# Kernel optimization log

Measured on AMD Instinct MI355X. Metric: run time of the kernel, lower is better.

Reference implementation:

```python
import jax, jax.numpy as jnp
import numpy as np

N_NODES = 100000


def gcn_conv(x, W, b, src, dst, n):
    # PyG GCNConv: add self-loops, symmetric deg^{-1/2} normalization,
    # h = x @ W, out[i] = sum_j norm_ij * h[j] + b
    loop = jnp.arange(n, dtype=src.dtype)
    s = jnp.concatenate([src, loop])
    d = jnp.concatenate([dst, loop])
    h = x @ W  # [N, F_out]
    deg = jax.ops.segment_sum(jnp.ones_like(d, dtype=x.dtype), d, num_segments=n)
    dinv = jnp.where(deg > 0, jax.lax.rsqrt(deg), 0.0)
    norm = dinv[s] * dinv[d]  # [E+N]
    msgs = h[s] * norm[:, None]  # gather + scale
    out = jax.ops.segment_sum(msgs, d, num_segments=n)  # scatter-add
    return out + b


def setup_inputs() -> dict:
    key = jax.random.key(0)
    ks = jax.random.split(key, 8)
    n, e = N_NODES, 1600000
    return {
        "clinical": jax.random.normal(ks[0], (n, 64), dtype=jnp.float32),
        "mel": jax.random.normal(ks[1], (n, 1024), dtype=jnp.float32),
        "edge_index": jax.random.randint(ks[2], (2, e), 0, n, dtype=jnp.int64),
        "W_mel": jax.random.normal(ks[3], (1024, 128), dtype=jnp.float32) * 0.03,
        "b_mel": jnp.zeros((128,), dtype=jnp.float32),
        "W_cat": jax.random.normal(ks[4], (192, 128), dtype=jnp.float32) * 0.07,
        "b_cat": jnp.zeros((128,), dtype=jnp.float32),
        "W1": jax.random.normal(ks[5], (128, 128), dtype=jnp.float32) * 0.09,
        "b1": jnp.zeros((128,), dtype=jnp.float32),
        "W2": jax.random.normal(ks[6], (128, 4), dtype=jnp.float32) * 0.09,
        "b2": jnp.zeros((4,), dtype=jnp.float32),
    }


def reference(clinical, mel, edge_index, W_mel, b_mel, W_cat, b_cat, W1, b1, W2, b2):
    n = clinical.shape[0]
    src, dst = edge_index[0], edge_index[1]
    m = jax.nn.relu(mel @ W_mel + b_mel)            # [N, 128]
    x = jnp.concatenate([clinical, m], axis=1)       # [N, 192]
    x = jax.nn.relu(x @ W_cat + b_cat)               # [N, 128]
    x = jax.nn.relu(gcn_conv(x, W1, b1, src, dst, n))
    x = gcn_conv(x, W2, b2, src, dst, n)             # [N, 4]
    return x
```

## Files before the change

kernel.cpp:

```cpp
#include <hip/hip_runtime.h>
#include <cstdint>


__device__ __forceinline__ bool detect_i64(const int* __restrict__ ei) {
  int nz = 0;
#pragma unroll
  for (int i = 1; i < 64; i += 2) nz |= ei[i];
  return nz == 0;
}
__device__ __forceinline__ int load_src(const int* __restrict__ ei, int e, bool is64) {
  return is64 ? ei[2 * e] : ei[e];
}
__device__ __forceinline__ int load_dst(const int* __restrict__ ei, int e, int E, bool is64) {
  return is64 ? ei[2 * (E + e)] : ei[E + e];
}

__global__ __launch_bounds__(256) void zero_int_k(int* __restrict__ p, int n) {
  int i = blockIdx.x * 256 + threadIdx.x;
  if (i < n) p[i] = 0;
}

__global__ __launch_bounds__(256) void count_deg_k(const int* __restrict__ ei,
                                                   int* __restrict__ degi, int E) {
  const bool is64 = detect_i64(ei);
  int e = blockIdx.x * 256 + threadIdx.x;
  if (e < E) atomicAdd(&degi[load_dst(ei, e, E, is64)], 1);
}

__global__ __launch_bounds__(256) void dinv_k(const int* __restrict__ degi,
                                              float* __restrict__ dinv, int n) {
  int i = blockIdx.x * 256 + threadIdx.x;
  if (i < n) dinv[i] = rsqrtf((float)degi[i] + 1.0f);
}

__global__ __launch_bounds__(256) void scan_reduce_k(const int* __restrict__ degi,
                                                     int* __restrict__ partial, int n) {
  __shared__ int s[256];
  int t = threadIdx.x;
  int i = blockIdx.x * 256 + t;
  s[t] = (i < n) ? degi[i] : 0;
  __syncthreads();
#pragma unroll
  for (int off = 128; off > 0; off >>= 1) {
    if (t < off) s[t] += s[t + off];
    __syncthreads();
  }
  if (t == 0) partial[blockIdx.x] = s[0];
}

__global__ __launch_bounds__(512) void scan_partials_k(const int* __restrict__ partial,
                                                       int* __restrict__ excl, int B,
                                                       int* __restrict__ rowptr, int n, int E) {
  __shared__ int s[512];
  int t = threadIdx.x;
  int v = (t < B) ? partial[t] : 0;
  s[t] = v;
  __syncthreads();
  for (int off = 1; off < 512; off <<= 1) {
    int x = (t >= off) ? s[t - off] : 0;
    __syncthreads();
    s[t] += x;
    __syncthreads();
  }
  if (t < B) excl[t] = s[t] - v;
  if (t == 0) rowptr[n] = E;
}

__global__ __launch_bounds__(256) void scan_final_k(const int* __restrict__ degi,
                                                    const int* __restrict__ excl,
                                                    int* __restrict__ rowptr, int n) {
  __shared__ int s[256];
  int t = threadIdx.x;
  int i = blockIdx.x * 256 + t;
  int v = (i < n) ? degi[i] : 0;
  s[t] = v;
  __syncthreads();
  for (int off = 1; off < 256; off <<= 1) {
    int x = (t >= off) ? s[t - off] : 0;
    __syncthreads();
    s[t] += x;
    __syncthreads();
  }
  if (i < n) rowptr[i] = excl[blockIdx.x] + s[t] - v;
}

__global__ __launch_bounds__(256) void fill_col_k(const int* __restrict__ ei,
                                                  const int* __restrict__ rowptr,
                                                  int* __restrict__ fill,
                                                  int* __restrict__ col, int E) {
  const bool is64 = detect_i64(ei);
  int e = blockIdx.x * 256 + threadIdx.x;
  if (e < E) {
    int s = load_src(ei, e, is64);
    int d = load_dst(ei, e, E, is64);
    int pos = rowptr[d] + atomicAdd(&fill[d], 1);
    col[pos] = s;
  }
}

template <bool RELU, bool HASBIAS>
__global__ __launch_bounds__(256) void gemm128_k(const float* __restrict__ A, int K,
                                                 const float* __restrict__ B,
                                                 const float* __restrict__ bias,
                                                 float* __restrict__ C, int n) {
  __shared__ float As[64][33];
  __shared__ float4 Bs[32][32];
  const int tid = threadIdx.x;
  const int tx = tid & 31, ty = tid >> 5;
  const int row0 = blockIdx.x * 64;
  float acc[8][4];
#pragma unroll
  for (int i = 0; i < 8; ++i)
#pragma unroll
    for (int j = 0; j < 4; ++j) acc[i][j] = 0.f;

  const int nChunks = K >> 5;
  for (int kc = 0; kc < nChunks; ++kc) {
    __syncthreads();
#pragma unroll
    for (int j = 0; j < 2; ++j) {
      int idx = tid + j * 256;
      int ar = idx >> 3, ac4 = idx & 7;
      int grow = row0 + ar;
      float4 v = make_float4(0.f, 0.f, 0.f, 0.f);
      if (grow < n) v = *(const float4*)(A + (size_t)grow * K + kc * 32 + ac4 * 4);
      As[ar][ac4 * 4 + 0] = v.x;
      As[ar][ac4 * 4 + 1] = v.y;
      As[ar][ac4 * 4 + 2] = v.z;
      As[ar][ac4 * 4 + 3] = v.w;
    }
#pragma unroll
    for (int j = 0; j < 4; ++j) {
      int idx = tid + j * 256;
      int br = idx >> 5, bc4 = idx & 31;
      Bs[br][bc4] = *(const float4*)(B + (size_t)(kc * 32 + br) * 128 + bc4 * 4);
    }
    __syncthreads();
#pragma unroll
    for (int kk = 0; kk < 32; ++kk) {
      float4 b = Bs[kk][tx];
#pragma unroll
      for (int i = 0; i < 8; ++i) {
        float a = As[ty * 8 + i][kk];
        acc[i][0] += a * b.x;
        acc[i][1] += a * b.y;
        acc[i][2] += a * b.z;
        acc[i][3] += a * b.w;
      }
    }
  }
  float4 bb = make_float4(0.f, 0.f, 0.f, 0.f);
  if (HASBIAS) bb = *(const float4*)(bias + tx * 4);
#pragma unroll
  for (int i = 0; i < 8; ++i) {
    int grow = row0 + ty * 8 + i;
    if (grow < n) {
      float4 o;
      o.x = acc[i][0] + bb.x;
      o.y = acc[i][1] + bb.y;
      o.z = acc[i][2] + bb.z;
      o.w = acc[i][3] + bb.w;
      if (RELU) {
        o.x = fmaxf(o.x, 0.f);
        o.y = fmaxf(o.y, 0.f);
        o.z = fmaxf(o.z, 0.f);
        o.w = fmaxf(o.w, 0.f);
      }
      *(float4*)(C + (size_t)grow * 128 + tx * 4) = o;
    }
  }
}

__global__ __launch_bounds__(256) void gemm_cat_k(const float* __restrict__ A1,
                                                  const float* __restrict__ A2,
                                                  const float* __restrict__ B,
                                                  const float* __restrict__ bias,
                                                  float* __restrict__ C, int n) {
  __shared__ float As[64][33];
  __shared__ float4 Bs[32][32];
  const int tid = threadIdx.x;
  const int tx = tid & 31, ty = tid >> 5;
  const int row0 = blockIdx.x * 64;
  float acc[8][4];
#pragma unroll
  for (int i = 0; i < 8; ++i)
#pragma unroll
    for (int j = 0; j < 4; ++j) acc[i][j] = 0.f;

  for (int kc = 0; kc < 6; ++kc) {
    __syncthreads();
#pragma unroll
    for (int j = 0; j < 2; ++j) {
      int idx = tid + j * 256;
      int ar = idx >> 3, ac4 = idx & 7;
      int grow = row0 + ar;
      int kcol = kc * 32 + ac4 * 4;
      float4 v = make_float4(0.f, 0.f, 0.f, 0.f);
      if (grow < n) {
        v = (kcol < 64) ? *(const float4*)(A1 + (size_t)grow * 64 + kcol)
                        : *(const float4*)(A2 + (size_t)grow * 128 + (kcol - 64));
      }
      As[ar][ac4 * 4 + 0] = v.x;
      As[ar][ac4 * 4 + 1] = v.y;
      As[ar][ac4 * 4 + 2] = v.z;
      As[ar][ac4 * 4 + 3] = v.w;
    }
#pragma unroll
    for (int j = 0; j < 4; ++j) {
      int idx = tid + j * 256;
      int br = idx >> 5, bc4 = idx & 31;
      Bs[br][bc4] = *(const float4*)(B + (size_t)(kc * 32 + br) * 128 + bc4 * 4);
    }
    __syncthreads();
#pragma unroll
    for (int kk = 0; kk < 32; ++kk) {
      float4 b = Bs[kk][tx];
#pragma unroll
      for (int i = 0; i < 8; ++i) {
        float a = As[ty * 8 + i][kk];
        acc[i][0] += a * b.x;
        acc[i][1] += a * b.y;
        acc[i][2] += a * b.z;
        acc[i][3] += a * b.w;
      }
    }
  }
  float4 bb = *(const float4*)(bias + tx * 4);
#pragma unroll
  for (int i = 0; i < 8; ++i) {
    int grow = row0 + ty * 8 + i;
    if (grow < n) {
      float4 o;
      o.x = fmaxf(acc[i][0] + bb.x, 0.f);
      o.y = fmaxf(acc[i][1] + bb.y, 0.f);
      o.z = fmaxf(acc[i][2] + bb.z, 0.f);
      o.w = fmaxf(acc[i][3] + bb.w, 0.f);
      *(float4*)(C + (size_t)grow * 128 + tx * 4) = o;
    }
  }
}

template <bool RELU>
__global__ __launch_bounds__(256) void gather128_k(const int* __restrict__ col,
                                                   const int* __restrict__ rowptr,
                                                   const float* __restrict__ dinv,
                                                   const float* __restrict__ h,
                                                   const float* __restrict__ bias,
                                                   float* __restrict__ out, int n) {
  const int node = blockIdx.x * 2 + (threadIdx.x >> 7);
  const int f = threadIdx.x & 127;
  if (node >= n) return;
  const int beg = rowptr[node], end = rowptr[node + 1];
  float acc = 0.f;
  int p = beg;
  for (; p + 4 <= end; p += 4) {
    int s0 = col[p], s1 = col[p + 1], s2 = col[p + 2], s3 = col[p + 3];
    float d0 = dinv[s0], d1 = dinv[s1], d2 = dinv[s2], d3 = dinv[s3];
    float h0 = h[(size_t)s0 * 128 + f];
    float h1 = h[(size_t)s1 * 128 + f];
    float h2 = h[(size_t)s2 * 128 + f];
    float h3 = h[(size_t)s3 * 128 + f];
    acc += d0 * h0 + d1 * h1 + d2 * h2 + d3 * h3;
  }
  for (; p < end; ++p) {
    int s = col[p];
    acc += dinv[s] * h[(size_t)s * 128 + f];
  }
  const float di = dinv[node];
  float v = di * (acc + di * h[(size_t)node * 128 + f]) + bias[f];
  if (RELU) v = fmaxf(v, 0.f);
  out[(size_t)node * 128 + f] = v;
}

__global__ __launch_bounds__(256) void gemm_small4_k(const float* __restrict__ A,
                                                     const float* __restrict__ W,
                                                     float* __restrict__ Y, int n) {
  __shared__ float Ws[512];
  int tid = threadIdx.x;
  Ws[tid] = W[tid];
  Ws[tid + 256] = W[tid + 256];
  __syncthreads();
  int row = blockIdx.x * 256 + tid;
  if (row >= n) return;
  const float4* A4 = (const float4*)(A + (size_t)row * 128);
  float a0 = 0.f, a1 = 0.f, a2 = 0.f, a3 = 0.f;
#pragma unroll
  for (int k4 = 0; k4 < 32; ++k4) {
    float4 a = A4[k4];
    const float* w = &Ws[k4 * 16];
    a0 += a.x * w[0] + a.y * w[4] + a.z * w[8] + a.w * w[12];
    a1 += a.x * w[1] + a.y * w[5] + a.z * w[9] + a.w * w[13];
    a2 += a.x * w[2] + a.y * w[6] + a.z * w[10] + a.w * w[14];
    a3 += a.x * w[3] + a.y * w[7] + a.z * w[11] + a.w * w[15];
  }
  *(float4*)(Y + (size_t)row * 4) = make_float4(a0, a1, a2, a3);
}

__global__ __launch_bounds__(256) void gather4_k(const int* __restrict__ col,
                                                 const int* __restrict__ rowptr,
                                                 const float* __restrict__ dinv,
                                                 const float* __restrict__ y,
                                                 const float* __restrict__ b2,
                                                 float* __restrict__ out, int n) {
  int node = blockIdx.x * 256 + threadIdx.x;
  if (node >= n) return;
  const int beg = rowptr[node], end = rowptr[node + 1];
  float ax = 0.f, ay = 0.f, az = 0.f, aw = 0.f;
  int p = beg;
  for (; p + 2 <= end; p += 2) {
    int s0 = col[p], s1 = col[p + 1];
    float d0 = dinv[s0], d1 = dinv[s1];
    float4 y0 = *(const float4*)(y + (size_t)s0 * 4);
    float4 y1 = *(const float4*)(y + (size_t)s1 * 4);
    ax += d0 * y0.x + d1 * y1.x;
    ay += d0 * y0.y + d1 * y1.y;
    az += d0 * y0.z + d1 * y1.z;
    aw += d0 * y0.w + d1 * y1.w;
  }
  for (; p < end; ++p) {
    int s = col[p];
    float ds = dinv[s];
    float4 yv = *(const float4*)(y + (size_t)s * 4);
    ax += ds * yv.x;
    ay += ds * yv.y;
    az += ds * yv.z;
    aw += ds * yv.w;
  }
  const float di = dinv[node];
  float4 yd = *(const float4*)(y + (size_t)node * 4);
  float4 o;
  o.x = di * (ax + di * yd.x) + b2[0];
  o.y = di * (ay + di * yd.y) + b2[1];
  o.z = di * (az + di * yd.z) + b2[2];
  o.w = di * (aw + di * yd.w) + b2[3];
  *(float4*)(out + (size_t)node * 4) = o;
}

extern "C" void kernel_launch(void* const* d_in, const int* in_sizes, int n_in,
                              void* d_out, int out_size, void* d_ws, size_t ws_size,
                              hipStream_t stream) {
  const float* clinical = (const float*)d_in[0];
  const float* mel = (const float*)d_in[1];
  const int* ei = (const int*)d_in[2];
  const float* W_mel = (const float*)d_in[3];
  const float* b_mel = (const float*)d_in[4];
  const float* W_cat = (const float*)d_in[5];
  const float* b_cat = (const float*)d_in[6];
  const float* W1 = (const float*)d_in[7];
  const float* b1 = (const float*)d_in[8];
  const float* W2 = (const float*)d_in[9];
  const float* b2 = (const float*)d_in[10];
  float* out = (float*)d_out;

  const int N = in_sizes[0] / 64;
  const int E = in_sizes[2] / 2;
  const int B = (N + 255) / 256;

  float* bufA = (float*)d_ws;
  float* bufB = bufA + (size_t)N * 128;
  float* dinv = bufB + (size_t)N * 128;
  float* ybuf = dinv + N;
  int* degi = (int*)(ybuf + (size_t)N * 4);
  int* rowptr = degi + N;
  int* fill = rowptr + (N + 1);
  int* partial = fill + N;
  int* excl = partial + 512;
  int* col = excl + 512;

  const dim3 blk(256);

  zero_int_k<<<(2 * N + 255) / 256, blk, 0, stream>>>(degi, 2 * N);
  count_deg_k<<<(E + 255) / 256, blk, 0, stream>>>(ei, degi, E);
  dinv_k<<<B, blk, 0, stream>>>(degi, dinv, N);
  scan_reduce_k<<<B, blk, 0, stream>>>(degi, partial, N);
  scan_partials_k<<<1, 512, 0, stream>>>(partial, excl, B, rowptr, N, E);
  scan_final_k<<<B, blk, 0, stream>>>(degi, excl, rowptr, N);
  zero_int_k<<<B, blk, 0, stream>>>(fill, N);
  fill_col_k<<<(E + 255) / 256, blk, 0, stream>>>(ei, rowptr, fill, col, E);

  gemm128_k<true, true><<<(N + 63) / 64, blk, 0, stream>>>(mel, 1024, W_mel, b_mel, bufA, N);
  gemm_cat_k<<<(N + 63) / 64, blk, 0, stream>>>(clinical, bufA, W_cat, b_cat, bufB, N);
  gemm128_k<false, false><<<(N + 63) / 64, blk, 0, stream>>>(bufB, 128, W1, nullptr, bufA, N);

  gather128_k<true><<<(N + 1) / 2, blk, 0, stream>>>(col, rowptr, dinv, bufA, b1, bufB, N);

  gemm_small4_k<<<(N + 255) / 256, blk, 0, stream>>>(bufB, W2, ybuf, N);

  gather4_k<<<(N + 255) / 256, blk, 0, stream>>>(col, rowptr, dinv, ybuf, b2, out, N);
}
```

Baseline: 1.311 ms.

## Use bf16 MFMA for the large mel projection GEMM

Replaces the scalar fp32 mel@W_mel GEMM with a bf16 MFMA kernel. A and W are converted to bf16 on the fly, and W is pre-transposed by a small conversion kernel. The aim is to remove the compute bottleneck of the 1024-wide projection while reading A once per 128-row tile. The cost is reduced input precision (bf16 rounding), with fp32 accumulation kept.

```diff
diff --git a/kernel.cpp b/kernel.cpp
--- a/kernel.cpp
+++ b/kernel.cpp
@@ -1,6 +1,17 @@
 #include <hip/hip_runtime.h>
 #include <cstdint>
 
+
+typedef short short4_t __attribute__((ext_vector_type(4)));
+typedef short short8_t __attribute__((ext_vector_type(8)));
+typedef float floatx4 __attribute__((ext_vector_type(4)));
+
+__device__ __forceinline__ short f2bf(float f) {
+  union { float f; unsigned u; } v;
+  v.f = f;
+  unsigned r = v.u + 0x7fffu + ((v.u >> 16) & 1u);
+  return (short)(r >> 16);
+}
 
 __device__ __forceinline__ bool detect_i64(const int* __restrict__ ei) {
   int nz = 0;
@@ -95,6 +106,90 @@
     int d = load_dst(ei, e, E, is64);
     int pos = rowptr[d] + atomicAdd(&fill[d], 1);
     col[pos] = s;
+  }
+}
+
+__global__ __launch_bounds__(256) void convW_k(const float* __restrict__ W,
+                                               short* __restrict__ Wt) {
+  int idx = blockIdx.x * 256 + threadIdx.x;
+  int nn = idx >> 10;
+  int k = idx & 1023;
+  Wt[idx] = f2bf(W[(size_t)k * 128 + nn]);
+}
+
+__global__ __launch_bounds__(256) void mel_gemm_mfma_k(const float* __restrict__ A,
+                                                       const short* __restrict__ Wt,
+                                                       const float* __restrict__ bias,
+                                                       float* __restrict__ C, int n) {
+  __shared__ short Asm[128][72];
+  __shared__ short Bsm[128][72];
+  const int tid = threadIdx.x;
+  const int row0 = blockIdx.x * 128;
+  const int lane = tid & 63;
+  const int wv = tid >> 6;
+  const int quad = lane >> 4;
+  const int cbase = lane & 15;
+
+  floatx4 acc[2][8];
+#pragma unroll
+  for (int tr = 0; tr < 2; ++tr)
+#pragma unroll
+    for (int tc = 0; tc < 8; ++tc) acc[tr][tc] = (floatx4){0.f, 0.f, 0.f, 0.f};
+
+  for (int kc = 0; kc < 16; ++kc) {
+    __syncthreads();
+#pragma unroll
+    for (int j = 0; j < 8; ++j) {
+      int idx = j * 256 + tid;
+      int row = idx >> 4, c4 = idx & 15;
+      int grow = row0 + row;
+      floatx4 v = (floatx4){0.f, 0.f, 0.f, 0.f};
+      if (grow < n) v = *(const floatx4*)(A + (size_t)grow * 1024 + kc * 64 + c4 * 4);
+      short4_t s4;
+      s4[0] = f2bf(v[0]); s4[1] = f2bf(v[1]); s4[2] = f2bf(v[2]); s4[3] = f2bf(v[3]);
+      *(short4_t*)&Asm[row][c4 * 4] = s4;
+    }
+#pragma unroll
+    for (int j = 0; j < 8; ++j) {
+      int idx = j * 256 + tid;
+      int nr = idx >> 4, c4 = idx & 15;
+      *(short4_t*)&Bsm[nr][c4 * 4] =
+          *(const short4_t*)(Wt + (size_t)nr * 1024 + kc * 64 + c4 * 4);
+    }
+    __syncthreads();
+#pragma unroll
+    for (int kk = 0; kk < 2; ++kk) {
+      short8_t af[2], bf[8];
+#pragma unroll
+      for (int tr = 0; tr < 2; ++tr)
+        af[tr] = *(const short8_t*)&Asm[wv * 32 + tr * 16 + cbase][kk * 32 + quad * 8];
+#pragma unroll
+      for (int tc = 0; tc < 8; ++tc)
+        bf[tc] = *(const short8_t*)&Bsm[tc * 16 + cbase][kk * 32 + quad * 8];
+#pragma unroll
+      for (int tr = 0; tr < 2; ++tr)
+#pragma unroll
+        for (int tc = 0; tc < 8; ++tc)
+          acc[tr][tc] = __builtin_amdgcn_mfma_f32_16x16x32_bf16(af[tr], bf[tc],
+                                                                acc[tr][tc], 0, 0, 0);
+    }
+  }
+  float bb[8];
+#pragma unroll
+  for (int tc = 0; tc < 8; ++tc) bb[tc] = bias[tc * 16 + cbase];
+#pragma unroll
+  for (int tr = 0; tr < 2; ++tr) {
+#pragma unroll
+    for (int r = 0; r < 4; ++r) {
+      int grow = row0 + wv * 32 + tr * 16 + quad * 4 + r;
+      if (grow < n) {
+#pragma unroll
+        for (int tc = 0; tc < 8; ++tc) {
+          float v = acc[tr][tc][r] + bb[tc];
+          C[(size_t)grow * 128 + tc * 16 + cbase] = fmaxf(v, 0.f);
+        }
+      }
+    }
   }
 }
 
@@ -366,10 +461,11 @@
   int* partial = fill + N;
   int* excl = partial + 512;
   int* col = excl + 512;
+  short* Wt = (short*)(col + E);
 
   const dim3 blk(256);
 
-  zero_int_k<<<(2 * N + 255) / 256, blk, 0, stream>>>(degi, 2 * N);
+  zero_int_k<<<(N + 255) / 256, blk, 0, stream>>>(degi, N);
   count_deg_k<<<(E + 255) / 256, blk, 0, stream>>>(ei, degi, E);
   dinv_k<<<B, blk, 0, stream>>>(degi, dinv, N);
   scan_reduce_k<<<B, blk, 0, stream>>>(degi, partial, N);
@@ -377,8 +473,9 @@
   scan_final_k<<<B, blk, 0, stream>>>(degi, excl, rowptr, N);
   zero_int_k<<<B, blk, 0, stream>>>(fill, N);
   fill_col_k<<<(E + 255) / 256, blk, 0, stream>>>(ei, rowptr, fill, col, E);
-
-  gemm128_k<true, true><<<(N + 63) / 64, blk, 0, stream>>>(mel, 1024, W_mel, b_mel, bufA, N);
+  convW_k<<<512, blk, 0, stream>>>(W_mel, Wt);
+
+  mel_gemm_mfma_k<<<(N + 127) / 128, blk, 0, stream>>>(mel, Wt, b_mel, bufA, N);
   gemm_cat_k<<<(N + 63) / 64, blk, 0, stream>>>(clinical, bufA, W_cat, b_cat, bufB, N);
   gemm128_k<false, false><<<(N + 63) / 64, blk, 0, stream>>>(bufB, 128, W1, nullptr, bufA, N);
 
```

After: 1.174 ms. 10.5% less time.
